# Performance work log

Hardware: AMD Instinct MI355X
Metric: run time of the kernel (lower is better)

The kernel has to match this reference:

```python
import jax, jax.numpy as jnp
import numpy as np


def _knn(coords, k):
    # coords: [N, 3]. Returns indices of the k nearest neighbors (self excluded): [N, k]
    sq = jnp.sum(coords * coords, axis=1)
    d2 = sq[:, None] + sq[None, :] - 2.0 * (coords @ coords.T)  # [N, N]
    n = coords.shape[0]
    d2 = jnp.where(jnp.eye(n, dtype=bool), jnp.inf, d2)  # loop=False: no self edges
    _, idx = jax.lax.top_k(-d2, k)
    return idx


def setup_inputs() -> dict:
    key = jax.random.key(0)
    ks = jax.random.split(key, 7)
    B, N, C = 8, 4096, 6
    feats = jax.random.normal(ks[0], (B, N, C), dtype=jnp.float32)
    # Glorot-ish scaled weights; PyG GCNConv lin has no bias, bias added post-aggregation.
    W1 = jax.random.normal(ks[1], (6, 64), dtype=jnp.float32) * (1.0 / np.sqrt(6))
    b1 = jnp.zeros((64,), dtype=jnp.float32)
    W2 = jax.random.normal(ks[2], (64, 128), dtype=jnp.float32) * (1.0 / np.sqrt(64))
    b2 = jnp.zeros((128,), dtype=jnp.float32)
    Wf = jax.random.normal(ks[3], (128, 128), dtype=jnp.float32) * (1.0 / np.sqrt(128))
    bf = jnp.zeros((128,), dtype=jnp.float32)
    return {"feats": feats, "W1": W1, "b1": b1, "W2": W2, "b2": b2,
            "Wf": Wf, "bf": bf, "k": 16}


def reference(feats, W1, b1, W2, b2, Wf, bf, k):
    # feats: [B, N, C]; coords = first 3 channels.
    coords = feats[..., :3]
    nbr = jax.vmap(lambda c: _knn(c, k))(coords)  # [B, N, k]
    inv_deg = 1.0 / (k + 1)  # every node has exactly k in-edges + self loop (uniform sym norm)
    x = feats
    for W, b in ((W1, b1), (W2, b2)):
        h = x @ W  # [B, N, H]
        nb = jax.vmap(lambda hb, ib: hb[ib])(h, nbr)  # gather neighbor feats: [B, N, k, H]
        x = jax.nn.relu((nb.sum(axis=2) + h) * inv_deg + b)  # GCN aggregate + bias + ReLU
    return x @ Wf + bf  # [B, N, out_dim]
```

## Files before the change

### kernel.cpp

```cpp
#include <hip/hip_runtime.h>
#include <cstdint>
#include <cstddef>

#define NPTS 4096
#define KNN  16
#define INV_DEG (1.0f / 17.0f)
#define CAP  48
#define TS   512

typedef unsigned long long u64;
typedef unsigned int u32;
typedef float v2f __attribute__((ext_vector_type(2)));

#define RAWSENT 0x7F800000FFFFFFFFull

__device__ __forceinline__ float unmapmono(u32 m) {
  u32 u = (m & 0x80000000u) ? (m ^ 0x80000000u) : ~m;
  return __uint_as_float(u);
}

__global__ __launch_bounds__(512) void knn_kernel(const float* __restrict__ feats,
                                                  const float* __restrict__ W1,
                                                  const float* __restrict__ b1,
                                                  int* __restrict__ nbr,
                                                  float* __restrict__ x1) {
#pragma clang fp contract(off)
  __shared__ float4 sc[TS];
  __shared__ u64 sbuf[8][2][64];

  const int b = blockIdx.x >> 8;
  const int pbase = (blockIdx.x & 255) * 16;
  const float* fb = feats + (size_t)b * NPTS * 6;
  const int wave = threadIdx.x >> 6;
  const int lane = threadIdx.x & 63;

  int ip[2];
  float xi[2], yi[2], zi[2], sqi[2], tau[2];
  u64 slot[2];
  int cnt[2];
#pragma unroll
  for (int p = 0; p < 2; ++p) {
    ip[p] = pbase + wave * 2 + p;
    const float* fr = fb + (size_t)ip[p] * 6;
    xi[p] = fr[0]; yi[p] = fr[1]; zi[p] = fr[2];
    sqi[p] = __fadd_rn(__fadd_rn(__fmul_rn(xi[p], xi[p]), __fmul_rn(yi[p], yi[p])),
                       __fmul_rn(zi[p], zi[p]));
    tau[p] = __uint_as_float(0x7f800000u);
    slot[p] = ~0ull;
    cnt[p] = 0;
  }

  auto flush = [&](int p) {
    u64* wb = &sbuf[wave][p][0];
    if (lane >= cnt[p] && lane < CAP) wb[lane] = RAWSENT;
    if (lane < KNN) wb[CAP + lane] = slot[p];
    u64 myk = wb[lane];
    if (lane < CAP) {
      u32 hi = (u32)(myk >> 32);
      hi ^= ((u32)((int)hi >> 31) | 0x80000000u);
      myk = ((u64)hi << 32) | (u32)myk;
      if ((u32)myk == (u32)ip[p]) myk = ~0ull;
      wb[lane] = myk;
    }
    int rank = 0;
#pragma unroll
    for (int m = 0; m < 64; m += 4) {
      u64 k0 = wb[m], k1 = wb[m + 1], k2 = wb[m + 2], k3 = wb[m + 3];
      rank += (int)(k0 < myk) + (int)(k1 < myk) + (int)(k2 < myk) + (int)(k3 < myk);
    }
    if (rank < KNN) wb[rank] = myk;
    u64 s15 = wb[15];
    if (lane < KNN) slot[p] = wb[lane];
    tau[p] = unmapmono((u32)(s15 >> 32));
    cnt[p] = 0;
  };

  for (int tb = 0; tb < NPTS; tb += TS) {
    __syncthreads();
    for (int t = threadIdx.x; t < TS; t += 512) {
      const float* fr = fb + (size_t)(tb + t) * 6;
      const float x = fr[0], y = fr[1], z = fr[2];
      const float sq = __fadd_rn(__fadd_rn(__fmul_rn(x, x), __fmul_rn(y, y)),
                                 __fmul_rn(z, z));
      float4 c; c.x = x; c.y = y; c.z = z; c.w = sq;
      sc[t] = c;
    }
    __syncthreads();

    for (int jb0 = 0; jb0 < TS; jb0 += 64) {
      const int tl = jb0 + lane;
      const int j = tb + tl;
      const float4 c = sc[tl];
      const v2f cx2 = {c.x, c.x}, cy2 = {c.y, c.y}, cz2 = {c.z, c.z},
                sq2 = {c.w, c.w};
      v2f X = {xi[0], xi[1]};
      v2f Y = {yi[0], yi[1]};
      v2f Z = {zi[0], zi[1]};
      v2f SQ = {sqi[0], sqi[1]};
      v2f dot = X * cx2;
      dot = __builtin_elementwise_fma(Y, cy2, dot);
      dot = __builtin_elementwise_fma(Z, cz2, dot);
      v2f two = {2.0f, 2.0f};
      v2f d2v = (SQ + sq2) - two * dot;
      float d2s[2] = {d2v.x, d2v.y};
#pragma unroll
      for (int p = 0; p < 2; ++p) {
        const bool pred = d2s[p] <= tau[p];
        const u64 bal = __ballot(pred);
        if (bal) {
          const int npass = __popcll(bal);
          if (cnt[p] + npass > CAP) flush(p);
          const int pos = cnt[p] + (int)__builtin_amdgcn_mbcnt_hi(
                                        (u32)(bal >> 32),
                                        __builtin_amdgcn_mbcnt_lo((u32)bal, 0));
          const u64 key = ((u64)__float_as_uint(d2s[p]) << 32) | (u32)j;
          if (npass <= CAP) {
            if (pred) sbuf[wave][p][pos] = key;
            cnt[p] += npass;
          } else {
            if (pred && pos < CAP) sbuf[wave][p][pos] = key;
            cnt[p] = CAP;
            flush(p);
            if (pred && pos >= CAP) sbuf[wave][p][pos - CAP] = key;
            cnt[p] = npass - CAP;
          }
        }
      }
    }
  }
#pragma unroll
  for (int p = 0; p < 2; ++p) flush(p);

  float* fsc = (float*)&sbuf[wave][0][0];
  float w1r[6];
#pragma unroll
  for (int k = 0; k < 6; ++k) w1r[k] = W1[k * 64 + lane];
  const float b1r = b1[lane];

#pragma unroll
  for (int p = 0; p < 2; ++p) {
    const int n = b * NPTS + ip[p];
    const int row = (lane < KNN) ? (int)(u32)slot[p] : ip[p];
    if (lane < KNN)
      nbr[(size_t)n * KNN + lane] = row;
    if (lane < 17) {
      const float* fr = fb + (size_t)row * 6;
      float2 r0 = *(const float2*)(fr);
      float2 r1 = *(const float2*)(fr + 2);
      float2 r2 = *(const float2*)(fr + 4);
      fsc[lane * 6 + 0] = r0.x; fsc[lane * 6 + 1] = r0.y;
      fsc[lane * 6 + 2] = r1.x; fsc[lane * 6 + 3] = r1.y;
      fsc[lane * 6 + 4] = r2.x; fsc[lane * 6 + 5] = r2.y;
    }
    __syncthreads();
    if (lane < 6) {
      float s = 0.f;
#pragma unroll
      for (int t = 0; t < 17; ++t) s += fsc[t * 6 + lane];
      fsc[102 + lane] = s;
    }
    __syncthreads();
    float s = 0.f;
#pragma unroll
    for (int k = 0; k < 6; ++k) s = fmaf(fsc[102 + k], w1r[k], s);
    x1[(size_t)n * 64 + lane] = fmaxf(fmaf(s, INV_DEG, b1r), 0.f);
    __syncthreads();
  }
}

__global__ __launch_bounds__(256) void enc2_kernel(const float* __restrict__ x1,
                                                   const int* __restrict__ nbr,
                                                   const float* __restrict__ W2,
                                                   const float* __restrict__ b2,
                                                   float* __restrict__ x2) {
  __shared__ float a1s[32][64];
  __shared__ v2f w2s[64][64];
  const int tid = threadIdx.x;
  const int n0 = blockIdx.x * 32;
  const int gb = n0 & ~(NPTS - 1);

#pragma unroll
  for (int i = 0; i < 16; ++i) {
    const int e = tid + 256 * i;
    const int k = e >> 6, l = e & 63;
    v2f w;
    w.x = W2[k * 128 + l];
    w.y = W2[k * 128 + 64 + l];
    w2s[k][l] = w;
  }
#pragma unroll
  for (int r = 0; r < 2; ++r) {
    const int p = r * 16 + (tid >> 4), c4 = tid & 15;
    const int n = n0 + p;
    const int* nb = nbr + (size_t)n * KNN;
    float4 s = ((const float4*)(x1 + (size_t)n * 64))[c4];
#pragma unroll
    for (int t = 0; t < KNN; ++t) {
      float4 v = ((const float4*)(x1 + (size_t)(gb + nb[t]) * 64))[c4];
      s.x += v.x; s.y += v.y; s.z += v.z; s.w += v.w;
    }
    *((float4*)&a1s[p][c4 * 4]) = s;
  }
  __syncthreads();

  const int wave = tid >> 6, lane = tid & 63;
  const int p0 = wave * 8;
  const float bx = b2[lane], by = b2[lane + 64];
  v2f acc[8];
#pragma unroll
  for (int i = 0; i < 8; ++i) acc[i] = (v2f){0, 0};
  for (int k = 0; k < 64; k += 4) {
    float4 a[8];
#pragma unroll
    for (int i = 0; i < 8; ++i) a[i] = *(const float4*)&a1s[p0 + i][k];
#pragma unroll
    for (int kk = 0; kk < 4; ++kk) {
      const v2f w = w2s[k + kk][lane];
#pragma unroll
      for (int i = 0; i < 8; ++i) {
        const float e = kk == 0 ? a[i].x : kk == 1 ? a[i].y : kk == 2 ? a[i].z
                                                                      : a[i].w;
        v2f v = {e, e};
        acc[i] = __builtin_elementwise_fma(v, w, acc[i]);
      }
    }
  }
#pragma unroll
  for (int pi = 0; pi < 8; ++pi) {
    float* row = x2 + (size_t)(n0 + p0 + pi) * 128;
    row[lane] = fmaxf(fmaf(acc[pi].x, INV_DEG, bx), 0.f);
    row[lane + 64] = fmaxf(fmaf(acc[pi].y, INV_DEG, by), 0.f);
  }
}

__global__ __launch_bounds__(256) void enc3_kernel(const float* __restrict__ x2,
                                                   const float* __restrict__ Wf,
                                                   const float* __restrict__ bf,
                                                   float* __restrict__ out) {
  __shared__ float xs[32 * 128];
  __shared__ float part[2][32][128];
  const int tid = threadIdx.x;
  const int n0 = blockIdx.x * 32;

#pragma unroll
  for (int i = 0; i < 4; ++i) {
    const int e = tid + 256 * i;
    ((float4*)xs)[e] = ((const float4*)(x2 + (size_t)n0 * 128))[e];
  }

  const int wave = tid >> 6, lane = tid & 63;
  const int kh = wave & 1, pg = wave >> 1;
  v2f w[64];
#pragma unroll
  for (int j = 0; j < 64; ++j) {
    const int k = kh * 64 + j;
    w[j].x = Wf[k * 128 + lane];
    w[j].y = Wf[k * 128 + 64 + lane];
  }
  __syncthreads();

  for (int pi = 0; pi < 16; ++pi) {
    const int p = pg * 16 + pi;
    v2f acc = {0, 0};
    for (int j = 0; j < 64; j += 4) {
      const float4 a = *(const float4*)&xs[p * 128 + kh * 64 + j];
#pragma unroll
      for (int jj = 0; jj < 4; ++jj) {
        const float e = jj == 0 ? a.x : jj == 1 ? a.y : jj == 2 ? a.z : a.w;
        v2f v = {e, e};
        acc = __builtin_elementwise_fma(v, w[j + jj], acc);
      }
    }
    part[kh][p][lane] = acc.x;
    part[kh][p][lane + 64] = acc.y;
  }
  __syncthreads();

#pragma unroll
  for (int i = 0; i < 16; ++i) {
    const int e = tid + 256 * i;
    const int p = e >> 7, c = e & 127;
    out[(size_t)(n0 + p) * 128 + c] = part[0][p][c] + part[1][p][c] + bf[c];
  }
}

extern "C" void kernel_launch(void* const* d_in, const int* in_sizes, int n_in,
                              void* d_out, int out_size, void* d_ws, size_t ws_size,
                              hipStream_t stream) {
  const float* feats = (const float*)d_in[0];
  const float* W1 = (const float*)d_in[1];
  const float* b1 = (const float*)d_in[2];
  const float* W2 = (const float*)d_in[3];
  const float* b2 = (const float*)d_in[4];
  const float* Wf = (const float*)d_in[5];
  const float* bf = (const float*)d_in[6];
  float* out = (float*)d_out;

  char* ws = (char*)d_ws;
  int* nbr = (int*)ws;
  float* x1 = (float*)(ws + (size_t)(2 << 20));
  float* x2 = out;

  knn_kernel<<<2048, 512, 0, stream>>>(feats, W1, b1, nbr, x1);
  enc2_kernel<<<1024, 256, 0, stream>>>(x1, nbr, W2, b2, x2);
  enc3_kernel<<<1024, 256, 0, stream>>>(x2, Wf, bf, out);
}
```

Before: 232.4 us.

## Fuse second GCN layer and final linear into one kernel; shrink KNN tile

Merges enc2 and enc3 into a single kernel over 16-point blocks. The layer-2 activations stay in shared memory, so the x2 round trip through global memory and one launch go away. W2 and Wf are streamed through a small shared tile in 16-row chunks instead of being held whole in shared memory or registers. The KNN tile size TS also drops from 512 to 256. Each block now re-reads both weight matrices with more syncthreads, and the TS change alters the KNN kernel's tiling.

```diff
diff --git a/kernel.cpp b/kernel.cpp
--- a/kernel.cpp
+++ b/kernel.cpp
@@ -6,7 +6,7 @@
 #define KNN  16
 #define INV_DEG (1.0f / 17.0f)
 #define CAP  48
-#define TS   512
+#define TS   256
 
 typedef unsigned long long u64;
 typedef unsigned int u32;
@@ -168,29 +168,23 @@
   }
 }
 
-__global__ __launch_bounds__(256) void enc2_kernel(const float* __restrict__ x1,
-                                                   const int* __restrict__ nbr,
-                                                   const float* __restrict__ W2,
-                                                   const float* __restrict__ b2,
-                                                   float* __restrict__ x2) {
-  __shared__ float a1s[32][64];
-  __shared__ v2f w2s[64][64];
+__global__ __launch_bounds__(256) void enc23_kernel(const float* __restrict__ x1,
+                                                    const int* __restrict__ nbr,
+                                                    const float* __restrict__ W2,
+                                                    const float* __restrict__ b2,
+                                                    const float* __restrict__ Wf,
+                                                    const float* __restrict__ bf,
+                                                    float* __restrict__ out) {
+  __shared__ float a1s[16][64];
+  __shared__ v2f wt[16][64];
+  __shared__ float xs[16][128];
   const int tid = threadIdx.x;
-  const int n0 = blockIdx.x * 32;
+  const int n0 = blockIdx.x * 16;
   const int gb = n0 & ~(NPTS - 1);
-
-#pragma unroll
-  for (int i = 0; i < 16; ++i) {
-    const int e = tid + 256 * i;
-    const int k = e >> 6, l = e & 63;
-    v2f w;
-    w.x = W2[k * 128 + l];
-    w.y = W2[k * 128 + 64 + l];
-    w2s[k][l] = w;
-  }
-#pragma unroll
-  for (int r = 0; r < 2; ++r) {
-    const int p = r * 16 + (tid >> 4), c4 = tid & 15;
+  const int wave = tid >> 6, lane = tid & 63;
+
+  {
+    const int p = tid >> 4, c4 = tid & 15;
     const int n = n0 + p;
     const int* nb = nbr + (size_t)n * KNN;
     float4 s = ((const float4*)(x1 + (size_t)n * 64))[c4];
@@ -201,86 +195,86 @@
     }
     *((float4*)&a1s[p][c4 * 4]) = s;
   }
-  __syncthreads();
-
-  const int wave = tid >> 6, lane = tid & 63;
-  const int p0 = wave * 8;
+
+  const int p0 = wave * 4;
   const float bx = b2[lane], by = b2[lane + 64];
-  v2f acc[8];
-#pragma unroll
-  for (int i = 0; i < 8; ++i) acc[i] = (v2f){0, 0};
-  for (int k = 0; k < 64; k += 4) {
-    float4 a[8];
-#pragma unroll
-    for (int i = 0; i < 8; ++i) a[i] = *(const float4*)&a1s[p0 + i][k];
-#pragma unroll
-    for (int kk = 0; kk < 4; ++kk) {
-      const v2f w = w2s[k + kk][lane];
-#pragma unroll
-      for (int i = 0; i < 8; ++i) {
-        const float e = kk == 0 ? a[i].x : kk == 1 ? a[i].y : kk == 2 ? a[i].z
-                                                                      : a[i].w;
-        v2f v = {e, e};
-        acc[i] = __builtin_elementwise_fma(v, w, acc[i]);
+
+  v2f acc[4];
+#pragma unroll
+  for (int i = 0; i < 4; ++i) acc[i] = (v2f){0, 0};
+  for (int kt = 0; kt < 64; kt += 16) {
+    __syncthreads();
+#pragma unroll
+    for (int i = 0; i < 4; ++i) {
+      const int e = tid + 256 * i;
+      const int k = e >> 6, l = e & 63;
+      v2f w;
+      w.x = W2[(kt + k) * 128 + l];
+      w.y = W2[(kt + k) * 128 + 64 + l];
+      wt[k][l] = w;
+    }
+    __syncthreads();
+    for (int kk = 0; kk < 16; kk += 4) {
+      float4 a[4];
+#pragma unroll
+      for (int i = 0; i < 4; ++i) a[i] = *(const float4*)&a1s[p0 + i][kt + kk];
+#pragma unroll
+      for (int j = 0; j < 4; ++j) {
+        const v2f w = wt[kk + j][lane];
+#pragma unroll
+        for (int i = 0; i < 4; ++i) {
+          const float e = j == 0 ? a[i].x : j == 1 ? a[i].y : j == 2 ? a[i].z
+                                                                     : a[i].w;
+          v2f v = {e, e};
+          acc[i] = __builtin_elementwise_fma(v, w, acc[i]);
+        }
       }
     }
   }
 #pragma unroll
-  for (int pi = 0; pi < 8; ++pi) {
-    float* row = x2 + (size_t)(n0 + p0 + pi) * 128;
-    row[lane] = fmaxf(fmaf(acc[pi].x, INV_DEG, bx), 0.f);
-    row[lane + 64] = fmaxf(fmaf(acc[pi].y, INV_DEG, by), 0.f);
-  }
-}
-
-__global__ __launch_bounds__(256) void enc3_kernel(const float* __restrict__ x2,
-                                                   const float* __restrict__ Wf,
-                                                   const float* __restrict__ bf,
-                                                   float* __restrict__ out) {
-  __shared__ float xs[32 * 128];
-  __shared__ float part[2][32][128];
-  const int tid = threadIdx.x;
-  const int n0 = blockIdx.x * 32;
-
-#pragma unroll
-  for (int i = 0; i < 4; ++i) {
-    const int e = tid + 256 * i;
-    ((float4*)xs)[e] = ((const float4*)(x2 + (size_t)n0 * 128))[e];
-  }
-
-  const int wave = tid >> 6, lane = tid & 63;
-  const int kh = wave & 1, pg = wave >> 1;
-  v2f w[64];
-#pragma unroll
-  for (int j = 0; j < 64; ++j) {
-    const int k = kh * 64 + j;
-    w[j].x = Wf[k * 128 + lane];
-    w[j].y = Wf[k * 128 + 64 + lane];
-  }
-  __syncthreads();
-
-  for (int pi = 0; pi < 16; ++pi) {
-    const int p = pg * 16 + pi;
-    v2f acc = {0, 0};
-    for (int j = 0; j < 64; j += 4) {
-      const float4 a = *(const float4*)&xs[p * 128 + kh * 64 + j];
-#pragma unroll
-      for (int jj = 0; jj < 4; ++jj) {
-        const float e = jj == 0 ? a.x : jj == 1 ? a.y : jj == 2 ? a.z : a.w;
-        v2f v = {e, e};
-        acc = __builtin_elementwise_fma(v, w[j + jj], acc);
+  for (int pi = 0; pi < 4; ++pi) {
+    xs[p0 + pi][lane] = fmaxf(fmaf(acc[pi].x, INV_DEG, bx), 0.f);
+    xs[p0 + pi][lane + 64] = fmaxf(fmaf(acc[pi].y, INV_DEG, by), 0.f);
+  }
+
+  v2f facc[4];
+#pragma unroll
+  for (int i = 0; i < 4; ++i) facc[i] = (v2f){0, 0};
+  for (int jt = 0; jt < 128; jt += 16) {
+    __syncthreads();
+#pragma unroll
+    for (int i = 0; i < 4; ++i) {
+      const int e = tid + 256 * i;
+      const int j = e >> 6, l = e & 63;
+      v2f w;
+      w.x = Wf[(jt + j) * 128 + l];
+      w.y = Wf[(jt + j) * 128 + 64 + l];
+      wt[j][l] = w;
+    }
+    __syncthreads();
+    for (int jj = 0; jj < 16; jj += 4) {
+      float4 a[4];
+#pragma unroll
+      for (int i = 0; i < 4; ++i) a[i] = *(const float4*)&xs[p0 + i][jt + jj];
+#pragma unroll
+      for (int j2 = 0; j2 < 4; ++j2) {
+        const v2f w = wt[jj + j2][lane];
+#pragma unroll
+        for (int i = 0; i < 4; ++i) {
+          const float e = j2 == 0 ? a[i].x : j2 == 1 ? a[i].y : j2 == 2 ? a[i].z
+                                                                        : a[i].w;
+          v2f v = {e, e};
+          facc[i] = __builtin_elementwise_fma(v, w, facc[i]);
+        }
       }
     }
-    part[kh][p][lane] = acc.x;
-    part[kh][p][lane + 64] = acc.y;
-  }
-  __syncthreads();
-
-#pragma unroll
-  for (int i = 0; i < 16; ++i) {
-    const int e = tid + 256 * i;
-    const int p = e >> 7, c = e & 127;
-    out[(size_t)(n0 + p) * 128 + c] = part[0][p][c] + part[1][p][c] + bf[c];
+  }
+  const float fx = bf[lane], fy = bf[lane + 64];
+#pragma unroll
+  for (int pi = 0; pi < 4; ++pi) {
+    float* row = out + (size_t)(n0 + p0 + pi) * 128;
+    row[lane] = facc[pi].x + fx;
+    row[lane + 64] = facc[pi].y + fy;
   }
 }
 
@@ -299,9 +293,7 @@
   char* ws = (char*)d_ws;
   int* nbr = (int*)ws;
   float* x1 = (float*)(ws + (size_t)(2 << 20));
-  float* x2 = out;
 
   knn_kernel<<<2048, 512, 0, stream>>>(feats, W1, b1, nbr, x1);
-  enc2_kernel<<<1024, 256, 0, stream>>>(x1, nbr, W2, b2, x2);
-  enc3_kernel<<<1024, 256, 0, stream>>>(x2, Wf, bf, out);
-}
+  enc23_kernel<<<2048, 256, 0, stream>>>(x1, nbr, W2, b2, Wf, bf, out);
+}
```

After: 239.9 us. 1.03x slower.
